# Performance work log

Measured on AMD Instinct MI355X. Metric: run time of the kernel, lower is better.

## Reference

```python
import jax, jax.numpy as jnp
import numpy as np

N = 50000      # nodes
E = 800000     # edges (before self-loops)
DIN, H1, H2, OUT = 128, 128, 64, 40
LN_EPS = 1e-5


def setup_inputs() -> dict:
    key = jax.random.key(0)
    ks = jax.random.split(key, 16)
    s = lambda d: 1.0 / np.sqrt(d)
    inp = {
        "x": jax.random.normal(ks[0], (N, DIN), jnp.float32),
        "edge_index": jax.random.randint(ks[1], (2, E), 0, N, dtype=jnp.int64),
        # GCNConv weights (applied as x @ W) and biases
        "W1": jax.random.normal(ks[2], (DIN, H1), jnp.float32) * s(DIN),
        "b1": jnp.zeros((H1,), jnp.float32),
        "W2": jax.random.normal(ks[3], (H1, H2), jnp.float32) * s(H1),
        "b2": jnp.zeros((H2,), jnp.float32),
        "W3": jax.random.normal(ks[4], (H2, H2), jnp.float32) * s(H2),
        "b3": jnp.zeros((H2,), jnp.float32),
        # LayerNorms
        "g1": jnp.ones((H1,), jnp.float32),
        "be1": jnp.zeros((H1,), jnp.float32),
        "g2": jnp.ones((H2,), jnp.float32),
        "be2": jnp.zeros((H2,), jnp.float32),
        # post_mp MLP head
        "Wp1": jax.random.normal(ks[5], (H2, H2), jnp.float32) * s(H2),
        "bp1": jnp.zeros((H2,), jnp.float32),
        "Wp2": jax.random.normal(ks[6], (H2, OUT), jnp.float32) * s(H2),
        "bp2": jnp.zeros((OUT,), jnp.float32),
    }
    return inp


def _layer_norm(x, g, b):
    mu = jnp.mean(x, axis=-1, keepdims=True)
    var = jnp.mean((x - mu) ** 2, axis=-1, keepdims=True)
    return (x - mu) * jax.lax.rsqrt(var + LN_EPS) * g + b


def _gcn(x, src, dst, norm, W, b):
    # PyG GCNConv: linear first, then normalized gather/scatter-add, bias last
    h = x @ W                                  # [N, H]
    msg = h[src] * norm[:, None]               # [E+N, H] gather
    out = jax.ops.segment_sum(msg, dst, num_segments=N)  # scatter-add
    return out + b


def reference(x, edge_index, W1, b1, W2, b2, W3, b3, g1, be1, g2, be2,
              Wp1, bp1, Wp2, bp2):
    loops = jnp.arange(N, dtype=edge_index.dtype)
    src = jnp.concatenate([edge_index[0], loops])  # add self-loops
    dst = jnp.concatenate([edge_index[1], loops])
    # symmetric normalization D^{-1/2} (A+I) D^{-1/2} (same graph all layers)
    deg = jax.ops.segment_sum(jnp.ones_like(src, dtype=x.dtype), dst,
                              num_segments=N)
    dinv = jnp.where(deg > 0, jax.lax.rsqrt(jnp.maximum(deg, 1.0)), 0.0)
    norm = dinv[src] * dinv[dst]

    h = _gcn(x, src, dst, norm, W1, b1)
    h = _layer_norm(jax.nn.relu(h), g1, be1)
    h = _gcn(h, src, dst, norm, W2, b2)
    h = _layer_norm(jax.nn.relu(h), g2, be2)
    emb = _gcn(h, src, dst, norm, W3, b3)      # emb = conv output, pre-ReLU
    h = jax.nn.relu(emb)
    h = (h @ Wp1 + bp1) @ Wp2 + bp2            # post_mp: two stacked Linears
    return emb, jax.nn.log_softmax(h, axis=1)
```

## Files before the change

### kernel.cpp

```cpp
#include <hip/hip_runtime.h>
#include <hip/hip_bf16.h>

#define DIN 128
#define HID1 128
#define HID2 64
#define OUTD 40
#define NCHUNK 128

typedef __attribute__((ext_vector_type(8))) short bf16x8;
typedef __attribute__((ext_vector_type(4))) float f32x4;

__device__ __forceinline__ float bf2f(unsigned int u) {
    union { unsigned int i; float f; } c;
    c.i = u << 16;
    return c.f;
}
__device__ __forceinline__ unsigned short f2bf(float f) {
    union { float f; unsigned int i; } c; c.f = f;
    unsigned int r = c.i + 0x7FFFu + ((c.i >> 16) & 1u);
    return (unsigned short)(r >> 16);
}
__device__ __forceinline__ unsigned int packbf(float lo, float hi) {
    return (unsigned int)f2bf(lo) | ((unsigned int)f2bf(hi) << 16);
}

__device__ __forceinline__ int get_src(const int* ei, int E, int e, int e64) {
    return e64 ? ei[2 * e] : ei[e];
}
__device__ __forceinline__ int get_dst(const int* ei, int E, int e, int e64) {
    return e64 ? ei[2 * (E + e)] : ei[E + e];
}

struct WCvt {
    const void* p[14];
    int sz[14];
    int off[14];
    int tobf[14];
    int cols[14];
};

__launch_bounds__(1024)
__global__ void posA_kernel(const unsigned short* __restrict__ xu,
                            const int* __restrict__ ei,
                            int* __restrict__ flags,
                            int* __restrict__ pos,
                            unsigned int* __restrict__ hist,
                            int E, int N) {
    __shared__ unsigned int h32[25000];
    __shared__ int sh2[2];
    const int NW = (N + 1) >> 1;
    const int b = blockIdx.x;
    const int t = threadIdx.x;
    if (b < NCHUNK) {
        if (t == 0) sh2[0] = 0;
        for (int w = t; w < NW; w += 1024) h32[w] = 0u;
        __syncthreads();
        int zodd = 0;
        for (int k = t; k < 1024; k += 1024)
            if (ei[2 * k + 1] == 0) zodd++;
        if (zodd) atomicAdd(&sh2[0], zodd);
        __syncthreads();
        const int e64 = (sh2[0] > 512) ? 1 : 0;
        const int CH = (E + NCHUNK - 1) / NCHUNK;
        const int lo = b * CH;
        int hi = lo + CH; if (hi > E) hi = E;
        for (int e = lo + t; e < hi; e += 1024) {
            int d = e64 ? ei[2 * (E + e)] : ei[E + e];
            if ((unsigned)d < (unsigned)N) {
                unsigned sh = (unsigned)(d & 1) << 4;
                unsigned old = atomicAdd(&h32[d >> 1], 1u << sh);
                pos[e] = (int)((old >> sh) & 0xffffu);
            } else {
                pos[e] = -1;
            }
        }
        __syncthreads();
        unsigned int* hb = hist + (size_t)b * NW;
        for (int w = t; w < NW; w += 1024) hb[w] = h32[w];
    } else {
        if (t < 2) sh2[t] = 0;
        __syncthreads();
        int bad = 0;
        for (int k = t; k < 2048; k += 1024) {
            float v = bf2f(xu[2 * k]);
            float a = fabsf(v);
            if (!(a <= 1e4f) || (v != 0.f && a < 1e-4f)) bad++;
        }
        int zodd = 0;
        for (int k = t; k < 1024; k += 1024)
            if (ei[2 * k + 1] == 0) zodd++;
        if (bad) atomicAdd(&sh2[0], bad);
        if (zodd) atomicAdd(&sh2[1], zodd);
        __syncthreads();
        if (t == 0) {
            flags[0] = (sh2[0] > 512) ? 1 : 0;
            flags[1] = (sh2[1] > 512) ? 1 : 0;
        }
    }
}

__launch_bounds__(256)
__global__ void phaseB_kernel(const unsigned int* __restrict__ hist,
                              unsigned int* __restrict__ basev,
                              int* __restrict__ cnt, int* __restrict__ bsum,
                              int N, int PB,
                              WCvt wc, unsigned short* __restrict__ wbf,
                              float* __restrict__ wf,
                              const int* __restrict__ flags) {
    __shared__ int red[256];
    const int NW = (N + 1) >> 1;
    int t = threadIdx.x;
    int blk = blockIdx.x;
    if (blk < PB) {
        int w = blk * 256 + t;
        unsigned run0 = 0, run1 = 0;
        if (w < NW) {
            #pragma unroll 4
            for (int b = 0; b < NCHUNK; ++b) {
                unsigned u = hist[(size_t)b * NW + w];
                basev[(size_t)b * NW + w] = (run0 & 0xffffu) | (run1 << 16);
                run0 += u & 0xffffu;
                run1 += u >> 16;
            }
            cnt[2 * w] = (int)run0;
            if (2 * w + 1 < N) cnt[2 * w + 1] = (int)run1;
        }
        int tot = 0;
        if (w < NW) tot = (int)run0 + ((2 * w + 1 < N) ? (int)run1 : 0);
        red[t] = tot;
        __syncthreads();
        #pragma unroll
        for (int off = 64; off >= 1; off >>= 1) {
            if ((t & 127) < off) red[t] += red[t + off];
            __syncthreads();
        }
        if (t == 0) bsum[2 * blk] = red[0];
        if (t == 128) bsum[2 * blk + 1] = red[128];
    } else {
        int xf32 = flags[0];
        int stride = (gridDim.x - PB) * 256;
        int tid = (blk - PB) * 256 + t;
        for (int a = 0; a < 14; ++a) {
            const float* pf = (const float*)wc.p[a];
            const unsigned short* pb = (const unsigned short*)wc.p[a];
            int n = wc.sz[a], off = wc.off[a], tobf = wc.tobf[a];
            int cols = wc.cols[a];
            int rows = tobf ? (n / cols) : 0;
            for (int i = tid; i < n; i += stride) {
                float v = xf32 ? pf[i] : bf2f(pb[i]);
                if (tobf) {
                    int k = i / cols, m = i % cols;
                    wbf[off + m * rows + k] = f2bf(v);
                } else {
                    wf[off + i] = v;
                }
            }
        }
    }
}

__global__ void scatter_kernel(const int* __restrict__ ei, const int* __restrict__ indptr,
                               const int* __restrict__ pos, const float* __restrict__ dinv,
                               const unsigned int* __restrict__ basev,
                               int2* __restrict__ csr_sn,
                               int E, int N, const int* __restrict__ flags) {
    int e64 = flags[1];
    int CH = (E + NCHUNK - 1) / NCHUNK;
    int NW = (N + 1) >> 1;
    int base = (blockIdx.x * blockDim.x + threadIdx.x) * 4;
    #pragma unroll
    for (int u = 0; u < 4; ++u) {
        int e = base + u;
        if (e < E) {
            int p = pos[e];
            if (p >= 0) {
                int bb = e / CH;
                int d = get_dst(ei, E, e, e64);
                int s = get_src(ei, E, e, e64);
                if ((unsigned)s >= (unsigned)N) s = 0;
                float nrm = dinv[s] * dinv[d];
                unsigned bw = basev[(size_t)bb * NW + (d >> 1)];
                int bval = (d & 1) ? (int)(bw >> 16) : (int)(bw & 0xffffu);
                int slot = indptr[d] + bval + p;
                csr_sn[slot] = make_int2(s, __float_as_int(nrm));
            }
        }
    }
}


template<typename AT>
__device__ __forceinline__ bf16x8 ld_afrag(const AT* p);
template<>
__device__ __forceinline__ bf16x8 ld_afrag<unsigned short>(const unsigned short* p) {
    return *(const bf16x8*)p;
}
template<>
__device__ __forceinline__ bf16x8 ld_afrag<float>(const float* p) {
    float4 a = *(const float4*)p;
    float4 b = *(const float4*)(p + 4);
    bf16x8 r;
    r[0] = (short)f2bf(a.x); r[1] = (short)f2bf(a.y);
    r[2] = (short)f2bf(a.z); r[3] = (short)f2bf(a.w);
    r[4] = (short)f2bf(b.x); r[5] = (short)f2bf(b.y);
    r[6] = (short)f2bf(b.z); r[7] = (short)f2bf(b.w);
    return r;
}

template<int K, int M, typename AT>
__device__ __forceinline__ void mm_body(const AT* __restrict__ A,
                                        const unsigned short* __restrict__ WT,
                                        unsigned short* __restrict__ C, int N,
                                        unsigned short (*Ws)[K + 8], int bx) {
    int tid = threadIdx.x;
    for (int idx = tid; idx < M * K / 8; idx += 256) {
        int r = idx / (K / 8), c8 = idx % (K / 8);
        *(uint4*)&Ws[r][c8 * 8] = *(const uint4*)&WT[r * K + c8 * 8];
    }
    __syncthreads();
    int w = tid >> 6, lane = tid & 63;
    int m = lane & 15, q = lane >> 4;
    int row_a = bx * 64 + w * 16 + m;
    if (row_a >= N) row_a = N - 1;
    const AT* arow = A + (size_t)row_a * K;
    f32x4 acc[M / 16];
    #pragma unroll
    for (int t = 0; t < M / 16; ++t) acc[t] = (f32x4){0.f, 0.f, 0.f, 0.f};
    #pragma unroll
    for (int ks = 0; ks < K / 32; ++ks) {
        int k0 = ks * 32 + q * 8;
        bf16x8 a = ld_afrag<AT>(arow + k0);
        #pragma unroll
        for (int t = 0; t < M / 16; ++t) {
            bf16x8 b = *(const bf16x8*)&Ws[t * 16 + m][k0];
            acc[t] = __builtin_amdgcn_mfma_f32_16x16x32_bf16(a, b, acc[t], 0, 0, 0);
        }
    }
    int rbase = bx * 64 + w * 16 + q * 4;
    #pragma unroll
    for (int reg = 0; reg < 4; ++reg) {
        int row = rbase + reg;
        if (row < N) {
            #pragma unroll
            for (int t = 0; t < M / 16; ++t)
                C[(size_t)row * M + t * 16 + m] = f2bf(acc[t][reg]);
        }
    }
}

template<int K, int M>
__launch_bounds__(256)
__global__ void emit_mm_kernel(const int* __restrict__ cnt, const int* __restrict__ bsum,
                               int* __restrict__ indptr, float* __restrict__ dinv,
                               int N, int NB,
                               const void* __restrict__ A,
                               const unsigned short* __restrict__ WT,
                               unsigned short* __restrict__ C,
                               const int* __restrict__ flags) {
    __shared__ unsigned short Ws[M][K + 8];
    int blk = blockIdx.x;
    int t = threadIdx.x;
    if (blk < NB) {
        int* part = (int*)&Ws[0][0];
        int* sh   = part + 256;
        part[t] = (t < NB) ? bsum[t] : 0;
        __syncthreads();
        for (int off = 1; off < 256; off <<= 1) {
            int v = (t >= off) ? part[t - off] : 0;
            __syncthreads();
            part[t] += v;
            __syncthreads();
        }
        int bbase = (blk > 0) ? part[blk - 1] : 0;
        int total = part[255];
        int i = blk * 256 + t;
        int c = (i < N) ? cnt[i] : 0;
        sh[t] = c;
        __syncthreads();
        for (int off = 1; off < 256; off <<= 1) {
            int v = (t >= off) ? sh[t - off] : 0;
            __syncthreads();
            sh[t] += v;
            __syncthreads();
        }
        if (i < N) {
            int excl = sh[t] - c + bbase;
            indptr[i] = excl;
            dinv[i] = 1.0f / sqrtf((float)(c + 1));
        }
        if (blk == NB - 1 && t == 0) indptr[N] = total;
    } else {
        int bx = blk - NB;
        if (flags[0]) mm_body<K, M, float>((const float*)A, WT, C, N, Ws, bx);
        else          mm_body<K, M, unsigned short>((const unsigned short*)A, WT, C, N, Ws, bx);
    }
}


template<int VPL>
__device__ __forceinline__ void gacc1(float* acc, const unsigned short* r, float n) {
    if constexpr (VPL == 8) {
        uint4 u = *(const uint4*)r;
        acc[0] += bf2f(u.x & 0xffffu) * n; acc[1] += bf2f(u.x >> 16) * n;
        acc[2] += bf2f(u.y & 0xffffu) * n; acc[3] += bf2f(u.y >> 16) * n;
        acc[4] += bf2f(u.z & 0xffffu) * n; acc[5] += bf2f(u.z >> 16) * n;
        acc[6] += bf2f(u.w & 0xffffu) * n; acc[7] += bf2f(u.w >> 16) * n;
    } else {
        uint2 u = *(const uint2*)r;
        acc[0] += bf2f(u.x & 0xffffu) * n; acc[1] += bf2f(u.x >> 16) * n;
        acc[2] += bf2f(u.y & 0xffffu) * n; acc[3] += bf2f(u.y >> 16) * n;
    }
}

template<int VPL>
__device__ __forceinline__ void gacc8(float* acc,
                                      const unsigned short* const* rp,
                                      const float* nv) {
    if constexpr (VPL == 8) {
        uint4 u[8];
        #pragma unroll
        for (int i = 0; i < 8; ++i) u[i] = *(const uint4*)rp[i];
        #pragma unroll
        for (int i = 0; i < 8; ++i) {
            float n = nv[i];
            acc[0] += bf2f(u[i].x & 0xffffu) * n; acc[1] += bf2f(u[i].x >> 16) * n;
            acc[2] += bf2f(u[i].y & 0xffffu) * n; acc[3] += bf2f(u[i].y >> 16) * n;
            acc[4] += bf2f(u[i].z & 0xffffu) * n; acc[5] += bf2f(u[i].z >> 16) * n;
            acc[6] += bf2f(u[i].w & 0xffffu) * n; acc[7] += bf2f(u[i].w >> 16) * n;
        }
    } else {
        uint2 u[8];
        #pragma unroll
        for (int i = 0; i < 8; ++i) u[i] = *(const uint2*)rp[i];
        #pragma unroll
        for (int i = 0; i < 8; ++i) {
            float n = nv[i];
            acc[0] += bf2f(u[i].x & 0xffffu) * n; acc[1] += bf2f(u[i].x >> 16) * n;
            acc[2] += bf2f(u[i].y & 0xffffu) * n; acc[3] += bf2f(u[i].y >> 16) * n;
        }
    }
}

template<int VPL, int H>
__device__ __forceinline__ void agg_node(float* acc,
                                         const unsigned short* __restrict__ h,
                                         const int* __restrict__ indptr,
                                         const int2* __restrict__ csr_sn,
                                         int nd, float di, int c0,
                                         int2 (*lsn), int idx) {
    #pragma unroll
    for (int v = 0; v < VPL; ++v) acc[v] = 0.f;
    gacc1<VPL>(acc, h + (size_t)nd * H + c0, di * di);
    int beg = indptr[nd], end = indptr[nd + 1];
    for (int base = beg; base < end; base += 32) {
        int m = end - base; if (m > 32) m = 32;
        lsn[idx]      = (idx < m)      ? csr_sn[base + idx]      : make_int2(0, 0);
        lsn[idx + 16] = (idx + 16 < m) ? csr_sn[base + idx + 16] : make_int2(0, 0);
        int rounds = (m + 7) >> 3;
        int j = 0;
        for (int rr = 0; rr < rounds; ++rr, j += 8) {
            const unsigned short* rp[8];
            float nv[8];
            #pragma unroll
            for (int i = 0; i < 8; ++i) {
                int2 e = lsn[j + i];
                rp[i] = h + (size_t)e.x * H + c0;
                nv[i] = __int_as_float(e.y);
            }
            gacc8<VPL>(acc, rp, nv);
        }
    }
}


template<int H, int M>
__launch_bounds__(256)
__global__ void aggmm_kernel(const unsigned short* __restrict__ h,
                             const int* __restrict__ indptr,
                             const int2* __restrict__ csr_sn,
                             const float* __restrict__ dinv,
                             const float* __restrict__ bias,
                             const float* __restrict__ gamma,
                             const float* __restrict__ beta,
                             const unsigned short* __restrict__ WT,
                             unsigned short* __restrict__ C, int N) {
    constexpr int VPL = H / 16;
    __shared__ unsigned short At[64][H + 8];
    __shared__ unsigned short Ws[M][H + 8];
    __shared__ int2 lsn[4][4][32];
    int tid = threadIdx.x;
    for (int i2 = tid; i2 < M * H / 8; i2 += 256) {
        int r = i2 / (H / 8), c8 = i2 % (H / 8);
        *(uint4*)&Ws[r][c8 * 8] = *(const uint4*)&WT[r * H + c8 * 8];
    }
    int w = tid >> 6;
    int lane = tid & 63;
    int g = lane >> 4;
    int idx = lane & 15;
    int c0 = idx * VPL;
    int grp = w * 4 + g;
    for (int nn = 0; nn < 4; ++nn) {
        int lrow = grp * 4 + nn;
        int node = blockIdx.x * 64 + lrow;
        int nd = (node < N) ? node : N - 1;
        float di = dinv[nd];
        float acc[VPL];
        agg_node<VPL, H>(acc, h, indptr, csr_sn, nd, di, c0, lsn[w][g], idx);
        #pragma unroll
        for (int v = 0; v < VPL; ++v) acc[v] = fmaxf(acc[v] + bias[c0 + v], 0.f);
        float s = 0.f, sq = 0.f;
        #pragma unroll
        for (int v = 0; v < VPL; ++v) { s += acc[v]; sq += acc[v] * acc[v]; }
        #pragma unroll
        for (int off = 8; off >= 1; off >>= 1) {
            s += __shfl_xor(s, off, 64);
            sq += __shfl_xor(sq, off, 64);
        }
        float mu = s * (1.0f / H);
        float var = fmaxf(sq * (1.0f / H) - mu * mu, 0.f);
        float inv = 1.0f / sqrtf(var + 1e-5f);
        #pragma unroll
        for (int v = 0; v < VPL; ++v)
            acc[v] = (acc[v] - mu) * inv * gamma[c0 + v] + beta[c0 + v];
        if constexpr (VPL == 8) {
            uint4 p;
            p.x = packbf(acc[0], acc[1]); p.y = packbf(acc[2], acc[3]);
            p.z = packbf(acc[4], acc[5]); p.w = packbf(acc[6], acc[7]);
            *(uint4*)&At[lrow][c0] = p;
        } else {
            uint2 p; p.x = packbf(acc[0], acc[1]); p.y = packbf(acc[2], acc[3]);
            *(uint2*)&At[lrow][c0] = p;
        }
    }
    __syncthreads();
    int m_ = lane & 15, q = lane >> 4;
    int lr = w * 16 + m_;
    f32x4 acc2[M / 16];
    #pragma unroll
    for (int t2 = 0; t2 < M / 16; ++t2) acc2[t2] = (f32x4){0.f, 0.f, 0.f, 0.f};
    #pragma unroll
    for (int ks = 0; ks < H / 32; ++ks) {
        int k0 = ks * 32 + q * 8;
        bf16x8 a = *(const bf16x8*)&At[lr][k0];
        #pragma unroll
        for (int t2 = 0; t2 < M / 16; ++t2) {
            bf16x8 b = *(const bf16x8*)&Ws[t2 * 16 + m_][k0];
            acc2[t2] = __builtin_amdgcn_mfma_f32_16x16x32_bf16(a, b, acc2[t2], 0, 0, 0);
        }
    }
    int rbase = blockIdx.x * 64 + w * 16 + q * 4;
    #pragma unroll
    for (int reg = 0; reg < 4; ++reg) {
        int row = rbase + reg;
        if (row < N) {
            #pragma unroll
            for (int t2 = 0; t2 < M / 16; ++t2)
                C[(size_t)row * M + t2 * 16 + m_] = f2bf(acc2[t2][reg]);
        }
    }
}


__launch_bounds__(256)
__global__ void agghead_kernel(const unsigned short* __restrict__ h,
                               const int* __restrict__ indptr,
                               const int2* __restrict__ csr_sn,
                               const float* __restrict__ dinv,
                               const float* __restrict__ bias,
                               const float* __restrict__ Wp1,
                               const float* __restrict__ bp1,
                               const float* __restrict__ Wp2,
                               const float* __restrict__ bp2,
                               void* __restrict__ d_out, int N,
                               const int* __restrict__ flags) {
    constexpr int VPL = 4;
    __shared__ float Est[64][68];
    __shared__ float W1s[64][64];
    __shared__ float Tst[64][68];
    __shared__ float W2s[64][OUTD];
    __shared__ float b1s[64];
    __shared__ float b2s[OUTD];
    __shared__ int2 lsn[4][4][32];
    int tid = threadIdx.x;
    int row0 = blockIdx.x * 64;
    for (int i = tid; i < 64 * 64; i += 256) W1s[i >> 6][i & 63] = Wp1[i];
    for (int i = tid; i < 64 * OUTD; i += 256) W2s[i / OUTD][i % OUTD] = Wp2[i];
    if (tid < 64) b1s[tid] = bp1[tid];
    if (tid < OUTD) b2s[tid] = bp2[tid];
    int w = tid >> 6;
    int lane = tid & 63;
    int g = lane >> 4;
    int idx = lane & 15;
    int c0 = idx * VPL;
    int grp = w * 4 + g;
    int xf32 = flags[0];
    for (int nn = 0; nn < 4; ++nn) {
        int lrow = grp * 4 + nn;
        int node = row0 + lrow;
        bool active = node < N;
        int nd = active ? node : N - 1;
        float di = dinv[nd];
        float acc[VPL];
        agg_node<VPL, HID2>(acc, h, indptr, csr_sn, nd, di, c0, lsn[w][g], idx);
        #pragma unroll
        for (int v = 0; v < VPL; ++v) acc[v] += bias[c0 + v];
        if (active) {
            if (xf32) {
                float* o = (float*)d_out + (size_t)node * HID2 + c0;
                *(float4*)o = make_float4(acc[0], acc[1], acc[2], acc[3]);
            } else {
                unsigned short* o = (unsigned short*)d_out + (size_t)node * HID2 + c0;
                ((unsigned int*)o)[0] = packbf(acc[0], acc[1]);
                ((unsigned int*)o)[1] = packbf(acc[2], acc[3]);
            }
        }
        #pragma unroll
        for (int v = 0; v < VPL; ++v)
            Est[c0 + v][lrow] = fmaxf(acc[v], 0.f);
    }
    __syncthreads();
    {
        int rg = tid >> 4, cg = tid & 15;
        int r = rg * 4, c = cg * 4;
        float acc[4][4];
        #pragma unroll
        for (int i = 0; i < 4; ++i)
            #pragma unroll
            for (int jj = 0; jj < 4; ++jj) acc[i][jj] = b1s[c + jj];
        #pragma unroll 4
        for (int k = 0; k < 64; ++k) {
            float4 a = *(const float4*)&Est[k][r];
            float4 wv = *(const float4*)&W1s[k][c];
            acc[0][0] += a.x * wv.x; acc[0][1] += a.x * wv.y; acc[0][2] += a.x * wv.z; acc[0][3] += a.x * wv.w;
            acc[1][0] += a.y * wv.x; acc[1][1] += a.y * wv.y; acc[1][2] += a.y * wv.z; acc[1][3] += a.y * wv.w;
            acc[2][0] += a.z * wv.x; acc[2][1] += a.z * wv.y; acc[2][2] += a.z * wv.z; acc[2][3] += a.z * wv.w;
            acc[3][0] += a.w * wv.x; acc[3][1] += a.w * wv.y; acc[3][2] += a.w * wv.z; acc[3][3] += a.w * wv.w;
        }
        #pragma unroll
        for (int i = 0; i < 4; ++i)
            #pragma unroll
            for (int jj = 0; jj < 4; ++jj) Tst[c + jj][r + i] = acc[i][jj];
    }
    __syncthreads();
    int row = tid >> 2, tc = tid & 3, o0 = tc * 10;
    int node = row0 + row;
    float u[10];
    #pragma unroll
    for (int o = 0; o < 10; ++o) u[o] = b2s[o0 + o];
    for (int c2 = 0; c2 < 64; ++c2) {
        float tv = Tst[c2][row];
        const float2* wp = (const float2*)&W2s[c2][o0];
        #pragma unroll
        for (int o2 = 0; o2 < 5; ++o2) {
            float2 wv = wp[o2];
            u[o2 * 2]     += tv * wv.x;
            u[o2 * 2 + 1] += tv * wv.y;
        }
    }
    float mx = u[0];
    #pragma unroll
    for (int o = 1; o < 10; ++o) mx = fmaxf(mx, u[o]);
    mx = fmaxf(mx, __shfl_xor(mx, 1, 64));
    mx = fmaxf(mx, __shfl_xor(mx, 2, 64));
    float sum = 0.f;
    #pragma unroll
    for (int o = 0; o < 10; ++o) sum += __expf(u[o] - mx);
    sum += __shfl_xor(sum, 1, 64);
    sum += __shfl_xor(sum, 2, 64);
    float lse = mx + __logf(sum);
    if (node < N) {
        if (xf32) {
            float* base = (float*)d_out + (size_t)N * HID2;
            float* op = base + (size_t)node * OUTD + o0;
            #pragma unroll
            for (int o = 0; o < 10; ++o) op[o] = u[o] - lse;
        } else {
            unsigned short* base = (unsigned short*)d_out + (size_t)N * HID2;
            unsigned int* op = (unsigned int*)(base + (size_t)node * OUTD + o0);
            #pragma unroll
            for (int o2 = 0; o2 < 5; ++o2)
                op[o2] = packbf(u[o2 * 2] - lse, u[o2 * 2 + 1] - lse);
        }
    }
}


extern "C" void kernel_launch(void* const* d_in, const int* in_sizes, int n_in,
                              void* d_out, int out_size, void* d_ws, size_t ws_size,
                              hipStream_t stream) {
    const unsigned short* xu = (const unsigned short*)d_in[0];
    const int*            ei = (const int*)d_in[1];

    const int N = in_sizes[0] / DIN;
    const int E = in_sizes[1] / 2;
    const int NW = (N + 1) / 2;

    size_t off = 0;
    auto take = [&](size_t bytes) {
        size_t cur = off;
        off += (bytes + 255) & ~(size_t)255;
        return cur;
    };
    char* ws = (char*)d_ws;
    int*   flags   = (int*)  (ws + take(256));
    int*   cnt     = (int*)  (ws + take((size_t)N * 4));
    float* dinv    = (float*)(ws + take((size_t)N * 4));
    int*   indptr  = (int*)  (ws + take((size_t)(N + 1) * 4));
    int*   pos     = (int*)  (ws + take((size_t)E * 4));
    int2*  csr_sn  = (int2*) (ws + take((size_t)E * 8));
    int*   bsum    = (int*)  (ws + take(((size_t)N / 256 + 4) * 4));
    unsigned int* hist  = (unsigned int*)(ws + take((size_t)NCHUNK * NW * 4));
    unsigned int* basev = (unsigned int*)(ws + take((size_t)NCHUNK * NW * 4));
    unsigned short* wbf = (unsigned short*)(ws + take(32768 * 2));
    float*          wf  = (float*)         (ws + take(8192 * 4));
    unsigned short* hbuf = (unsigned short*)(ws + take((size_t)N * DIN * 2));
    unsigned short* abuf = (unsigned short*)(ws + take((size_t)N * DIN * 2));
    (void)ws_size; (void)n_in; (void)out_size;

    const int TB = 256;
    dim3 blk(TB);
    const int NB = (N + 255) / 256;
    const int PB = (NW + 255) / 256;
    const int MMG = (N + 63) / 64;

    WCvt wc;
    int bfoff = 0, foff = 0;
    int offs[14];
    const int wcols[14] = {HID1, 0, HID2, 0, HID2, 0, 0, 0, 0, 0, 0, 0, 0, 0};
    for (int a = 0; a < 14; ++a) {
        int idx = a + 2;
        wc.p[a] = d_in[idx];
        wc.sz[a] = in_sizes[idx];
        int tobf = (idx == 2 || idx == 4 || idx == 6) ? 1 : 0;
        wc.tobf[a] = tobf;
        wc.cols[a] = tobf ? wcols[a] : 1;
        if (tobf) { wc.off[a] = bfoff; bfoff += in_sizes[idx]; }
        else      { wc.off[a] = foff;  foff  += in_sizes[idx]; }
        offs[a] = wc.off[a];
    }

    unsigned short* W1t = wbf + offs[0];
    unsigned short* W2t = wbf + offs[2];
    unsigned short* W3t = wbf + offs[4];
    float* b1f  = wf + offs[1];
    float* b2f  = wf + offs[3];
    float* b3f  = wf + offs[5];
    float* g1f  = wf + offs[6];
    float* be1f = wf + offs[7];
    float* g2f  = wf + offs[8];
    float* be2f = wf + offs[9];
    float* Wp1f = wf + offs[10];
    float* bp1f = wf + offs[11];
    float* Wp2f = wf + offs[12];
    float* bp2f = wf + offs[13];

    posA_kernel<<<dim3(NCHUNK + 1), dim3(1024), 0, stream>>>(
        xu, ei, flags, pos, hist, E, N);
    phaseB_kernel<<<dim3(PB + 64), blk, 0, stream>>>(
        hist, basev, cnt, bsum, N, PB, wc, wbf, wf, flags);
    emit_mm_kernel<DIN, HID1><<<dim3(NB + MMG), blk, 0, stream>>>(
        cnt, bsum, indptr, dinv, N, NB, d_in[0], W1t, hbuf, flags);
    scatter_kernel<<<dim3((E + 1023) / 1024), blk, 0, stream>>>(
        ei, indptr, pos, dinv, basev, csr_sn, E, N, flags);

    aggmm_kernel<HID1, HID2><<<dim3(MMG), blk, 0, stream>>>(
        hbuf, indptr, csr_sn, dinv, b1f, g1f, be1f, W2t, abuf, N);
    aggmm_kernel<HID2, HID2><<<dim3(MMG), blk, 0, stream>>>(
        abuf, indptr, csr_sn, dinv, b2f, g2f, be2f, W3t, hbuf, N);
    agghead_kernel<<<dim3(MMG), blk, 0, stream>>>(
        hbuf, indptr, csr_sn, dinv, b3f, Wp1f, bp1f, Wp2f, bp2f, d_out, N, flags);
}
```

Before: 276.0 us.

## Split fused aggregation+head kernel into separate aggregation and MLP head kernels

The last GCN aggregation is moved out of the fused agghead kernel into a standalone agg_kernel. It handles one node per 16-lane group, with 16 nodes per block over many more blocks, and writes a bf16 copy of the embedding to a scratch buffer alongside the output embedding. A separate head_kernel then reads that bf16 buffer, applies ReLU and runs the two linears and log_softmax. The aim is more parallelism and latency hiding in the gather phase, where previously each group walked 4 nodes serially inside a large-shared-memory block. The cost is an extra launch and an extra global round-trip of the embedding.

```diff
diff --git a/kernel.cpp b/kernel.cpp
--- a/kernel.cpp
+++ b/kernel.cpp
@@ -461,62 +461,106 @@
 }
 
 
+template<int H, bool RELU_LN, bool EMB>
 __launch_bounds__(256)
-__global__ void agghead_kernel(const unsigned short* __restrict__ h,
-                               const int* __restrict__ indptr,
-                               const int2* __restrict__ csr_sn,
-                               const float* __restrict__ dinv,
-                               const float* __restrict__ bias,
-                               const float* __restrict__ Wp1,
-                               const float* __restrict__ bp1,
-                               const float* __restrict__ Wp2,
-                               const float* __restrict__ bp2,
-                               void* __restrict__ d_out, int N,
-                               const int* __restrict__ flags) {
-    constexpr int VPL = 4;
+__global__ void agg_kernel(const unsigned short* __restrict__ h,
+                           const int* __restrict__ indptr,
+                           const int2* __restrict__ csr_sn,
+                           const float* __restrict__ dinv,
+                           const float* __restrict__ bias,
+                           const float* __restrict__ gamma,
+                           const float* __restrict__ beta,
+                           unsigned short* __restrict__ out,
+                           void* __restrict__ out_emb,
+                           int N, const int* __restrict__ flags) {
+    constexpr int VPL = H / 16;
+    __shared__ int2 lsn[4][4][32];
+    int w = threadIdx.x >> 6;
+    int lane = threadIdx.x & 63;
+    int g = lane >> 4;
+    int idx = lane & 15;
+    int node = blockIdx.x * 16 + w * 4 + g;
+    bool active = node < N;
+    int nd = active ? node : N - 1;
+    float di = dinv[nd];
+    int c0 = idx * VPL;
+    float acc[VPL];
+    agg_node<VPL, H>(acc, h, indptr, csr_sn, nd, di, c0, lsn[w][g], idx);
+    #pragma unroll
+    for (int v = 0; v < VPL; ++v) acc[v] += bias[c0 + v];
+    if constexpr (RELU_LN) {
+        #pragma unroll
+        for (int v = 0; v < VPL; ++v) acc[v] = fmaxf(acc[v], 0.f);
+        float s = 0.f, sq = 0.f;
+        #pragma unroll
+        for (int v = 0; v < VPL; ++v) { s += acc[v]; sq += acc[v] * acc[v]; }
+        #pragma unroll
+        for (int off = 8; off >= 1; off >>= 1) {
+            s += __shfl_xor(s, off, 64);
+            sq += __shfl_xor(sq, off, 64);
+        }
+        float mu = s * (1.0f / H);
+        float var = fmaxf(sq * (1.0f / H) - mu * mu, 0.f);
+        float inv = 1.0f / sqrtf(var + 1e-5f);
+        #pragma unroll
+        for (int v = 0; v < VPL; ++v)
+            acc[v] = (acc[v] - mu) * inv * gamma[c0 + v] + beta[c0 + v];
+    }
+    if (active) {
+        unsigned short* orow = out + (size_t)node * H + c0;
+        if constexpr (VPL == 8) {
+            uint4 p;
+            p.x = packbf(acc[0], acc[1]); p.y = packbf(acc[2], acc[3]);
+            p.z = packbf(acc[4], acc[5]); p.w = packbf(acc[6], acc[7]);
+            *(uint4*)orow = p;
+        } else {
+            uint2 p; p.x = packbf(acc[0], acc[1]); p.y = packbf(acc[2], acc[3]);
+            *(uint2*)orow = p;
+        }
+        if constexpr (EMB) {
+            if (flags[0]) {
+                float* o = (float*)out_emb + (size_t)node * H + c0;
+                #pragma unroll
+                for (int v4 = 0; v4 < VPL / 4; ++v4)
+                    *(float4*)(o + v4 * 4) = make_float4(acc[v4 * 4], acc[v4 * 4 + 1],
+                                                         acc[v4 * 4 + 2], acc[v4 * 4 + 3]);
+            } else {
+                unsigned short* o = (unsigned short*)out_emb + (size_t)node * H + c0;
+                #pragma unroll
+                for (int v2 = 0; v2 < VPL / 2; ++v2)
+                    ((unsigned int*)o)[v2] = packbf(acc[v2 * 2], acc[v2 * 2 + 1]);
+            }
+        }
+    }
+}
+
+
+__launch_bounds__(256)
+__global__ void head_kernel(const unsigned short* __restrict__ emb,
+                            const float* __restrict__ Wp1,
+                            const float* __restrict__ bp1,
+                            const float* __restrict__ Wp2,
+                            const float* __restrict__ bp2,
+                            void* __restrict__ d_out, int N,
+                            const int* __restrict__ flags) {
     __shared__ float Est[64][68];
     __shared__ float W1s[64][64];
     __shared__ float Tst[64][68];
     __shared__ float W2s[64][OUTD];
     __shared__ float b1s[64];
     __shared__ float b2s[OUTD];
-    __shared__ int2 lsn[4][4][32];
     int tid = threadIdx.x;
     int row0 = blockIdx.x * 64;
     for (int i = tid; i < 64 * 64; i += 256) W1s[i >> 6][i & 63] = Wp1[i];
     for (int i = tid; i < 64 * OUTD; i += 256) W2s[i / OUTD][i % OUTD] = Wp2[i];
     if (tid < 64) b1s[tid] = bp1[tid];
     if (tid < OUTD) b2s[tid] = bp2[tid];
-    int w = tid >> 6;
-    int lane = tid & 63;
-    int g = lane >> 4;
-    int idx = lane & 15;
-    int c0 = idx * VPL;
-    int grp = w * 4 + g;
-    int xf32 = flags[0];
-    for (int nn = 0; nn < 4; ++nn) {
-        int lrow = grp * 4 + nn;
-        int node = row0 + lrow;
-        bool active = node < N;
-        int nd = active ? node : N - 1;
-        float di = dinv[nd];
-        float acc[VPL];
-        agg_node<VPL, HID2>(acc, h, indptr, csr_sn, nd, di, c0, lsn[w][g], idx);
-        #pragma unroll
-        for (int v = 0; v < VPL; ++v) acc[v] += bias[c0 + v];
-        if (active) {
-            if (xf32) {
-                float* o = (float*)d_out + (size_t)node * HID2 + c0;
-                *(float4*)o = make_float4(acc[0], acc[1], acc[2], acc[3]);
-            } else {
-                unsigned short* o = (unsigned short*)d_out + (size_t)node * HID2 + c0;
-                ((unsigned int*)o)[0] = packbf(acc[0], acc[1]);
-                ((unsigned int*)o)[1] = packbf(acc[2], acc[3]);
-            }
-        }
-        #pragma unroll
-        for (int v = 0; v < VPL; ++v)
-            Est[c0 + v][lrow] = fmaxf(acc[v], 0.f);
+    for (int i = tid; i < 64 * 32; i += 256) {
+        int r = i >> 5, kk = i & 31;
+        int row = row0 + r;
+        unsigned int u = (row < N) ? *(const unsigned int*)&emb[(size_t)row * 64 + kk * 2] : 0u;
+        Est[kk * 2][r]     = fmaxf(bf2f(u & 0xffffu), 0.f);
+        Est[kk * 2 + 1][r] = fmaxf(bf2f(u >> 16), 0.f);
     }
     __syncthreads();
     {
@@ -569,7 +613,7 @@
     sum += __shfl_xor(sum, 2, 64);
     float lse = mx + __logf(sum);
     if (node < N) {
-        if (xf32) {
+        if (flags[0]) {
             float* base = (float*)d_out + (size_t)N * HID2;
             float* op = base + (size_t)node * OUTD + o0;
             #pragma unroll
@@ -667,6 +711,8 @@
         hbuf, indptr, csr_sn, dinv, b1f, g1f, be1f, W2t, abuf, N);
     aggmm_kernel<HID2, HID2><<<dim3(MMG), blk, 0, stream>>>(
         abuf, indptr, csr_sn, dinv, b2f, g2f, be2f, W3t, hbuf, N);
-    agghead_kernel<<<dim3(MMG), blk, 0, stream>>>(
-        hbuf, indptr, csr_sn, dinv, b3f, Wp1f, bp1f, Wp2f, bp2f, d_out, N, flags);
-}
+    agg_kernel<HID2, false, true><<<dim3((N + 15) / 16), blk, 0, stream>>>(
+        hbuf, indptr, csr_sn, dinv, b3f, nullptr, nullptr, abuf, d_out, N, flags);
+    head_kernel<<<dim3(MMG), blk, 0, stream>>>(
+        abuf, Wp1f, bp1f, Wp2f, bp2f, d_out, N, flags);
+}
```

After: 277.5 us. About the same (+0.6%).
